# Performance work log

Measured on AMD Instinct MI355X. Metric: run time of the kernel, lower is better.

Reference implementation:

```python
import jax, jax.numpy as jnp
import numpy as np

N_NODES = 100000
N_EDGES = 1_600_000
D_IN = 128
D_OUT = 128


def setup_inputs() -> dict:
    key = jax.random.key(0)
    k1, k2, k3 = jax.random.split(key, 3)
    input_matrix = jax.random.normal(k1, (N_NODES, D_IN), dtype=jnp.float32)
    adjacency_coo_matrix = jax.random.randint(k2, (2, N_EDGES), 0, N_NODES, dtype=jnp.int64)
    # xavier-uniform-style init for the weight matrix
    limit = float(np.sqrt(6.0 / (D_IN + D_OUT)))
    weights_matrix = jax.random.uniform(k3, (D_IN, D_OUT), dtype=jnp.float32, minval=-limit, maxval=limit)
    return {
        "input_matrix": input_matrix,
        "adjacency_coo_matrix": adjacency_coo_matrix,
        "weights_matrix": weights_matrix,
    }


def reference(input_matrix, adjacency_coo_matrix, weights_matrix):
    # Edge-wise gathers (the irregular-access pattern from the torch code)
    src_idx = adjacency_coo_matrix[0]
    dst_idx = adjacency_coo_matrix[1]
    neighbors = input_matrix[dst_idx]  # [E, D_IN] gather of neighbor features
    # Mean-aggregate neighbor features onto each src node
    agg = jax.ops.segment_sum(neighbors, src_idx, num_segments=N_NODES)  # [N, D_IN]
    deg = jax.ops.segment_sum(jnp.ones((neighbors.shape[0],), dtype=input_matrix.dtype),
                              src_idx, num_segments=N_NODES)  # [N]
    mean_agg = agg / jnp.maximum(deg, 1.0)[:, None]
    # Linear transform with the layer weight matrix
    out = mean_agg @ weights_matrix  # [N, D_OUT]
    return out
```

## Files before the change

### kernel.cpp

```cpp
#include <hip/hip_runtime.h>

#define NN 100000
#define NE 1600000
#define DD 128
#define CAP 60
#define SLICES 8
#define SLICE_N 12500

typedef __bf16 bf16x8 __attribute__((ext_vector_type(8)));
typedef float  f32x4  __attribute__((ext_vector_type(4)));

__device__ __forceinline__ unsigned int f2bf(float f) {
    unsigned int u = __float_as_uint(f);
    return (u + 0x7FFFu + ((u >> 16) & 1u)) >> 16;
}
__device__ __forceinline__ float bflo(unsigned int u) { return __uint_as_float(u << 16); }
__device__ __forceinline__ float bfhi(unsigned int u) { return __uint_as_float(u & 0xFFFF0000u); }

#define WLD 136
__global__ __launch_bounds__(256) void k_gemm_xw(const float* __restrict__ x,
                                                 const float* __restrict__ W,
                                                 unsigned short* __restrict__ y)
{
    __shared__ unsigned short Wl[DD * WLD];
    for (int idx = threadIdx.x; idx < DD * DD; idx += 256) {
        const int n = idx >> 7, k = idx & 127;
        Wl[n * WLD + k] = (unsigned short)f2bf(W[k * DD + n]);
    }
    __syncthreads();

    const int wave = threadIdx.x >> 6;
    const int lane = threadIdx.x & 63;
    const int quad = lane >> 4;
    const int l16  = lane & 15;
    const int mbase = blockIdx.x * 64 + wave * 16;
    const int m = mbase + l16;

    bf16x8 a[4];
    if (m < NN) {
        const float* arow = x + (size_t)m * DD + quad * 8;
        #pragma unroll
        for (int ks = 0; ks < 4; ++ks) {
            const float4 f0 = *(const float4*)(arow + ks * 32);
            const float4 f1 = *(const float4*)(arow + ks * 32 + 4);
            uint4 p;
            p.x = f2bf(f0.x) | (f2bf(f0.y) << 16);
            p.y = f2bf(f0.z) | (f2bf(f0.w) << 16);
            p.z = f2bf(f1.x) | (f2bf(f1.y) << 16);
            p.w = f2bf(f1.z) | (f2bf(f1.w) << 16);
            a[ks] = __builtin_bit_cast(bf16x8, p);
        }
    } else {
        const uint4 z = make_uint4(0, 0, 0, 0);
        #pragma unroll
        for (int ks = 0; ks < 4; ++ks) a[ks] = __builtin_bit_cast(bf16x8, z);
    }

    #pragma unroll
    for (int nt = 0; nt < 8; ++nt) {
        f32x4 c = {0.f, 0.f, 0.f, 0.f};
        const unsigned short* bcol = &Wl[(nt * 16 + l16) * WLD + quad * 8];
        #pragma unroll
        for (int ks = 0; ks < 4; ++ks) {
            const bf16x8 b = __builtin_bit_cast(bf16x8, *(const uint4*)(bcol + ks * 32));
            c = __builtin_amdgcn_mfma_f32_16x16x32_bf16(a[ks], b, c, 0, 0, 0);
        }
        #pragma unroll
        for (int r = 0; r < 4; ++r) {
            const int row = mbase + quad * 4 + r;
            if (row < NN)
                y[(size_t)row * DD + nt * 16 + l16] = (unsigned short)f2bf(c[r]);
        }
    }
}

__global__ __launch_bounds__(256) void k_fill2(const int* __restrict__ adj,
                                               int* __restrict__ cnt,
                                               int* __restrict__ edge_dst)
{
    const int slice = blockIdx.x & 7;
    const int w     = blockIdx.x >> 3;
    const int lo    = slice * SLICE_N;
    for (int e = w * 256 + threadIdx.x; e < NE; e += 128 * 256) {
        int src = adj[e];
        if ((unsigned)(src - lo) < (unsigned)SLICE_N) {
            int dst  = adj[NE + e];
            int slot = atomicAdd(&cnt[src], 1);
            if (slot < CAP) edge_dst[src * CAP + slot] = dst;
        }
    }
}

__global__ __launch_bounds__(256) void k_agg2(const unsigned short* __restrict__ y,
                                              const int* __restrict__ cnt,
                                              const int* __restrict__ edge_dst,
                                              float* __restrict__ out)
{
    const int n    = blockIdx.x * 4 + (threadIdx.x >> 6);
    const int lane = threadIdx.x & 63;
    const int eg   = lane >> 4;
    const int h    = lane & 15;
    int deg = cnt[n];
    if (deg > CAP) deg = CAP;
    const int* el = edge_dst + n * CAP;

    float acc[8] = {0.f,0.f,0.f,0.f,0.f,0.f,0.f,0.f};

    int i = eg;
    for (; i + 4 < deg; i += 8) {
        const int d0 = el[i];
        const int d1 = el[i + 4];
        const uint4 p0 = *(const uint4*)(y + (size_t)d0 * DD + h * 8);
        const uint4 p1 = *(const uint4*)(y + (size_t)d1 * DD + h * 8);
        acc[0] += bflo(p0.x); acc[1] += bfhi(p0.x);
        acc[2] += bflo(p0.y); acc[3] += bfhi(p0.y);
        acc[4] += bflo(p0.z); acc[5] += bfhi(p0.z);
        acc[6] += bflo(p0.w); acc[7] += bfhi(p0.w);
        acc[0] += bflo(p1.x); acc[1] += bfhi(p1.x);
        acc[2] += bflo(p1.y); acc[3] += bfhi(p1.y);
        acc[4] += bflo(p1.z); acc[5] += bfhi(p1.z);
        acc[6] += bflo(p1.w); acc[7] += bfhi(p1.w);
    }
    for (; i < deg; i += 4) {
        const int d0 = el[i];
        const uint4 p0 = *(const uint4*)(y + (size_t)d0 * DD + h * 8);
        acc[0] += bflo(p0.x); acc[1] += bfhi(p0.x);
        acc[2] += bflo(p0.y); acc[3] += bfhi(p0.y);
        acc[4] += bflo(p0.z); acc[5] += bfhi(p0.z);
        acc[6] += bflo(p0.w); acc[7] += bfhi(p0.w);
    }

    #pragma unroll
    for (int j = 0; j < 8; ++j) {
        acc[j] += __shfl_xor(acc[j], 16, 64);
        acc[j] += __shfl_xor(acc[j], 32, 64);
    }

    if (eg == 0) {
        const float inv = 1.0f / fmaxf((float)deg, 1.0f);
        float* o = out + (size_t)n * DD + h * 8;
        float4 w0 = {acc[0]*inv, acc[1]*inv, acc[2]*inv, acc[3]*inv};
        float4 w1 = {acc[4]*inv, acc[5]*inv, acc[6]*inv, acc[7]*inv};
        *(float4*)(o + 0) = w0;
        *(float4*)(o + 4) = w1;
    }
}

extern "C" void kernel_launch(void* const* d_in, const int* in_sizes, int n_in,
                              void* d_out, int out_size, void* d_ws, size_t ws_size,
                              hipStream_t stream) {
    const float* x   = (const float*)d_in[0];
    const int*   adj = (const int*)d_in[1];
    const float* W   = (const float*)d_in[2];
    float* out = (float*)d_out;

    unsigned short* y   = (unsigned short*)d_ws;
    int* cnt      = (int*)(y + (size_t)NN * DD);
    int* edge_dst = cnt + NN;

    hipMemsetAsync(cnt, 0, NN * sizeof(int), stream);
    k_fill2  <<<1024, 256, 0, stream>>>(adj, cnt, edge_dst);
    k_gemm_xw<<<(NN + 63) / 64, 256, 0, stream>>>(x, W, y);
    k_agg2   <<<NN / 4, 256, 0, stream>>>(y, cnt, edge_dst, out);
}
```

Baseline: 293.3 us.

## Fuse edge bucketing and XW GEMM into one launch with vectorized index loads

Merges the CSR-style fill kernel and the bf16 MFMA GEMM into a single launch, with the block index choosing which role a block plays. The two independent stages can then run concurrently and one launch boundary goes away. The fill path now reads source and destination indices as uint4 groups of four instead of one int at a time. CAP goes from 60 to 64 so each node's edge list is 256 bytes and aligned. The fused kernel reserves the GEMM's shared-memory tile even for fill blocks, which may lower occupancy for the atomic-heavy fill work.

```diff
diff --git a/kernel.cpp b/kernel.cpp
--- a/kernel.cpp
+++ b/kernel.cpp
@@ -3,9 +3,11 @@
 #define NN 100000
 #define NE 1600000
 #define DD 128
-#define CAP 60
+#define CAP 64
 #define SLICES 8
 #define SLICE_N 12500
+#define FILL_BLOCKS 1024
+#define GEMM_BLOCKS ((NN + 63) / 64)
 
 typedef __bf16 bf16x8 __attribute__((ext_vector_type(8)));
 typedef float  f32x4  __attribute__((ext_vector_type(4)));
@@ -18,11 +20,40 @@
 __device__ __forceinline__ float bfhi(unsigned int u) { return __uint_as_float(u & 0xFFFF0000u); }
 
 #define WLD 136
-__global__ __launch_bounds__(256) void k_gemm_xw(const float* __restrict__ x,
-                                                 const float* __restrict__ W,
-                                                 unsigned short* __restrict__ y)
+__global__ __launch_bounds__(256) void k_fused(const int* __restrict__ adj,
+                                               int* __restrict__ cnt,
+                                               int* __restrict__ edge_dst,
+                                               const float* __restrict__ x,
+                                               const float* __restrict__ W,
+                                               unsigned short* __restrict__ y)
 {
     __shared__ unsigned short Wl[DD * WLD];
+
+    if (blockIdx.x < FILL_BLOCKS) {
+        const int slice = blockIdx.x & 7;
+        const int w     = blockIdx.x >> 3;
+        const int lo    = slice * SLICE_N;
+        const uint4* src4 = (const uint4*)adj;
+        const uint4* dst4 = (const uint4*)(adj + NE);
+        const int ngroups = NE / 4;
+
+        for (int g = w * 256 + (int)threadIdx.x; g < ngroups; g += FILL_BLOCKS / 8 * 256) {
+            const uint4 s4 = src4[g];
+            const uint4 d4 = dst4[g];
+            #pragma unroll
+            for (int j = 0; j < 4; ++j) {
+                const int s = (j == 0) ? s4.x : (j == 1) ? s4.y : (j == 2) ? s4.z : s4.w;
+                const int d = (j == 0) ? d4.x : (j == 1) ? d4.y : (j == 2) ? d4.z : d4.w;
+                if ((unsigned)(s - lo) < (unsigned)SLICE_N) {
+                    int slot = atomicAdd(&cnt[s], 1);
+                    if (slot < CAP) edge_dst[(size_t)s * CAP + slot] = d;
+                }
+            }
+        }
+        return;
+    }
+
+    const int bid = blockIdx.x - FILL_BLOCKS;
     for (int idx = threadIdx.x; idx < DD * DD; idx += 256) {
         const int n = idx >> 7, k = idx & 127;
         Wl[n * WLD + k] = (unsigned short)f2bf(W[k * DD + n]);
@@ -33,7 +64,7 @@
     const int lane = threadIdx.x & 63;
     const int quad = lane >> 4;
     const int l16  = lane & 15;
-    const int mbase = blockIdx.x * 64 + wave * 16;
+    const int mbase = bid * 64 + wave * 16;
     const int m = mbase + l16;
 
     bf16x8 a[4];
@@ -74,23 +105,6 @@
     }
 }
 
-__global__ __launch_bounds__(256) void k_fill2(const int* __restrict__ adj,
-                                               int* __restrict__ cnt,
-                                               int* __restrict__ edge_dst)
-{
-    const int slice = blockIdx.x & 7;
-    const int w     = blockIdx.x >> 3;
-    const int lo    = slice * SLICE_N;
-    for (int e = w * 256 + threadIdx.x; e < NE; e += 128 * 256) {
-        int src = adj[e];
-        if ((unsigned)(src - lo) < (unsigned)SLICE_N) {
-            int dst  = adj[NE + e];
-            int slot = atomicAdd(&cnt[src], 1);
-            if (slot < CAP) edge_dst[src * CAP + slot] = dst;
-        }
-    }
-}
-
 __global__ __launch_bounds__(256) void k_agg2(const unsigned short* __restrict__ y,
                                               const int* __restrict__ cnt,
                                               const int* __restrict__ edge_dst,
@@ -102,7 +116,7 @@
     const int h    = lane & 15;
     int deg = cnt[n];
     if (deg > CAP) deg = CAP;
-    const int* el = edge_dst + n * CAP;
+    const int* el = edge_dst + (size_t)n * CAP;
 
     float acc[8] = {0.f,0.f,0.f,0.f,0.f,0.f,0.f,0.f};
 
@@ -154,12 +168,11 @@
     const float* W   = (const float*)d_in[2];
     float* out = (float*)d_out;
 
-    unsigned short* y   = (unsigned short*)d_ws;
+    unsigned short* y = (unsigned short*)d_ws;
     int* cnt      = (int*)(y + (size_t)NN * DD);
     int* edge_dst = cnt + NN;
 
     hipMemsetAsync(cnt, 0, NN * sizeof(int), stream);
-    k_fill2  <<<1024, 256, 0, stream>>>(adj, cnt, edge_dst);
-    k_gemm_xw<<<(NN + 63) / 64, 256, 0, stream>>>(x, W, y);
-    k_agg2   <<<NN / 4, 256, 0, stream>>>(y, cnt, edge_dst, out);
+    k_fused<<<FILL_BLOCKS + GEMM_BLOCKS, 256, 0, stream>>>(adj, cnt, edge_dst, x, W, y);
+    k_agg2 <<<NN / 4, 256, 0, stream>>>(y, cnt, edge_dst, out);
 }
```

Result: faster. 278.2 us (-5.1%).
